# Optimization experiments

Hardware: AMD Instinct MI355X
Metric: run time of the kernel (lower is better)

## Reference

```python
import jax, jax.numpy as jnp
import numpy as np

EMBED_DIM = 512
NUM_HEADS = 8
HEAD_DIM = EMBED_DIM // NUM_HEADS
QK_CH = 64  # hard-coded in the torch module


def setup_inputs() -> dict:
    key = jax.random.key(0)
    ks = jax.random.split(key, 9)
    B, C, H, W = 16, EMBED_DIM, 64, 64
    s = lambda k, shape, fan: jax.random.normal(k, shape, jnp.float32) * (1.0 / np.sqrt(fan))
    return {
        "x": jax.random.normal(ks[0], (B, C, H, W), jnp.float32),
        "Wq": s(ks[1], (QK_CH, C), C),
        "bq": jnp.zeros((QK_CH,), jnp.float32),
        "Wk": s(ks[2], (QK_CH, C), C),
        "bk": jnp.zeros((QK_CH,), jnp.float32),
        "Wv": s(ks[3], (C, C), C),
        "bv": jnp.zeros((C,), jnp.float32),
        "Wo": s(ks[4], (C, C), C),
        "bo": jnp.zeros((C,), jnp.float32),
    }


def reference(x, Wq, bq, Wk, bk, Wv, bv, Wo, bo):
    B, C, H, W = x.shape
    nh, hd = NUM_HEADS, HEAD_DIM
    HW = H * W
    # 1x1 convs == pointwise channel projections
    q = jnp.einsum('bchw,oc->bohw', x, Wq) + bq[None, :, None, None]   # [B,64,H,W]
    k = jnp.einsum('bchw,oc->bohw', x, Wk) + bk[None, :, None, None]   # [B,64,H,W]
    v = jnp.einsum('bchw,oc->bohw', x, Wv) + bv[None, :, None, None]   # [B,C,H,W]
    # split_heads: view(B, nh, -1, hd).permute(0,1,3,2)
    Lq = QK_CH * HW // C
    q = q.reshape(B, nh, Lq, hd).transpose(0, 1, 3, 2)   # [B,nh,hd,Lq]
    k = k.reshape(B, nh, Lq, hd).transpose(0, 1, 3, 2)   # [B,nh,hd,Lq]
    v = v.reshape(B, nh, HW, hd).transpose(0, 1, 3, 2)   # [B,nh,hd,HW]
    # scores: [B,nh,hd,hd], softmax over last dim
    scores = jnp.einsum('bhdl,bhel->bhde', q, k) / np.sqrt(hd).astype(np.float32)
    attn = jax.nn.softmax(scores, axis=-1)
    out = jnp.einsum('bhde,bhen->bhdn', attn, v)          # [B,nh,hd,HW]
    # permute(0,1,3,2).view(B,nh,hd,H,W).permute(0,2,1,3,4).view(B,C,H,W)
    out = out.transpose(0, 1, 3, 2).reshape(B, nh, hd, H, W)
    out = out.transpose(0, 2, 1, 3, 4).reshape(B, C, H, W)
    # output_linear on the flat view [B, HW, C] (plain reshape, as in torch)
    out = out.reshape(B, HW, C) @ Wo.T + bo
    return out.reshape(B, C, H, W)
```

## Files before the change

kernel.cpp:

```cpp
#include <hip/hip_runtime.h>
#include <hip/hip_bf16.h>


#define B_  16
#define C_  512
#define HW_ 4096
#define NO_ 640

typedef unsigned short u16;
typedef __attribute__((ext_vector_type(8))) short bh8;
typedef __attribute__((ext_vector_type(4))) float f32x4;

__device__ __forceinline__ float bf2f(u16 u) {
    unsigned v = ((unsigned)u) << 16;
    return __uint_as_float(v);
}
__device__ __forceinline__ u16 f2bf(float f) {
    unsigned u = __float_as_uint(f);
    unsigned r = (u + 0x7FFFu + ((u >> 16) & 1u)) >> 16;
    return (u16)r;
}

__device__ __forceinline__ void gl2lds(const u16* g, u16* l) {
    __builtin_amdgcn_global_load_lds(
        (const __attribute__((address_space(1))) unsigned int*)(const void*)g,
        (__attribute__((address_space(3))) unsigned int*)(void*)l, 16, 0, 0);
}

__global__ __launch_bounds__(256) void k_wcvt(
    const float* __restrict__ Wq, const float* __restrict__ Wk,
    const float* __restrict__ Wv, const float* __restrict__ Wo,
    u16* __restrict__ Wcat, u16* __restrict__ Wob)
{
    int idx = blockIdx.x * 256 + threadIdx.x;
    if (idx < NO_ * C_) {
        int o = idx >> 9, c = idx & 511;
        float v = (o < 64) ? Wq[o * C_ + c]
                : (o < 128) ? Wk[(o - 64) * C_ + c]
                : Wv[(size_t)(o - 128) * C_ + c];
        Wcat[idx] = f2bf(v);
    }
    int idx2 = idx - NO_ * C_;
    if (idx2 >= 0 && idx2 < C_ * C_) Wob[idx2] = f2bf(Wo[idx2]);
}

__global__ __launch_bounds__(256) void k_x2t(
    const float* __restrict__ x, u16* __restrict__ xT)
{
    __shared__ u16 T[32][33];
    const int t = threadIdx.x;
    const int s0 = blockIdx.x * 32, c0 = blockIdx.y * 32, b = blockIdx.z;
    const float* xb = x + ((size_t)b * C_ + c0) * HW_ + s0;
    {
        int c = t >> 3, s4 = (t & 7) * 4;
        float4 v = *(const float4*)(xb + (size_t)c * HW_ + s4);
        T[s4][c] = f2bf(v.x); T[s4 + 1][c] = f2bf(v.y);
        T[s4 + 2][c] = f2bf(v.z); T[s4 + 3][c] = f2bf(v.w);
    }
    __syncthreads();
    {
        int s = t >> 3, cb = (t & 7) * 4;
        ushort4 o;
        o.x = T[s][cb]; o.y = T[s][cb + 1]; o.z = T[s][cb + 2]; o.w = T[s][cb + 3];
        *(ushort4*)(xT + ((size_t)b * HW_ + s0 + s) * C_ + c0 + cb) = o;
    }
}

__global__ __launch_bounds__(256) void k_proj(
    const u16* __restrict__ Wcat, const u16* __restrict__ xT,
    const float* __restrict__ bq, const float* __restrict__ bk,
    const float* __restrict__ bv, u16* __restrict__ qkv)
{
    __shared__ u16 As[128 * 32];
    __shared__ u16 Bs[128 * 32];
    const int t = threadIdx.x;
    const int lane = t & 63, w = t >> 6;
    const int q = lane >> 4, ln = lane & 15;
    const int n0 = blockIdx.x * 128, m0 = blockIdx.y * 128, b = blockIdx.z;
    const u16* xTb = xT + (size_t)b * HW_ * C_;
    const int wm = (w >> 1) * 64, wn = (w & 1) * 64;
    const int srow = lane >> 2, scol = (lane & 3) * 8;

    f32x4 acc[4][4];
#pragma unroll
    for (int i = 0; i < 4; ++i)
#pragma unroll
        for (int j = 0; j < 4; ++j) acc[i][j] = (f32x4){0.f, 0.f, 0.f, 0.f};

    for (int k0 = 0; k0 < C_; k0 += 32) {
        __syncthreads();
#pragma unroll
        for (int i = 0; i < 2; ++i) {
            int rowblk = (i * 4 + w) * 16;
            gl2lds(Wcat + (size_t)(m0 + rowblk + srow) * C_ + k0 + scol, &As[rowblk * 32]);
            gl2lds(xTb  + (size_t)(n0 + rowblk + srow) * C_ + k0 + scol, &Bs[rowblk * 32]);
        }
        __syncthreads();
        bh8 af[4], bfv[4];
#pragma unroll
        for (int i = 0; i < 4; ++i) af[i]  = *(const bh8*)&As[(wm + i * 16 + ln) * 32 + q * 8];
#pragma unroll
        for (int j = 0; j < 4; ++j) bfv[j] = *(const bh8*)&Bs[(wn + j * 16 + ln) * 32 + q * 8];
#pragma unroll
        for (int i = 0; i < 4; ++i)
#pragma unroll
            for (int j = 0; j < 4; ++j)
                acc[i][j] = __builtin_amdgcn_mfma_f32_16x16x32_bf16(af[i], bfv[j], acc[i][j], 0, 0, 0);
    }

    u16* qb = qkv + (size_t)b * NO_ * HW_;
#pragma unroll
    for (int i = 0; i < 4; ++i) {
#pragma unroll
        for (int r = 0; r < 4; ++r) {
            int o = m0 + wm + i * 16 + q * 4 + r;
            float bia = (o < 64) ? bq[o] : (o < 128) ? bk[o - 64] : bv[o - 128];
#pragma unroll
            for (int j = 0; j < 4; ++j) {
                int s = n0 + wn + j * 16 + ln;
                qb[(size_t)o * HW_ + s] = f2bf(acc[i][j][r] + bia);
            }
        }
    }
}

__global__ __launch_bounds__(256) void k_scores(
    const u16* __restrict__ qkv, float* __restrict__ At)
{
    __shared__ float Ks[64][4];
    __shared__ float Ss[64 * 65];
    const int t = threadIdx.x;
    const int bh = blockIdx.x;
    const int b = bh >> 3, head = bh & 7;
    const int d = t & 63, eg = t >> 6;
    const u16* qbase = qkv + ((size_t)b * NO_ + 8 * head) * HW_;
    const u16* kbase = qkv + ((size_t)b * NO_ + 64 + 8 * head) * HW_;

    float acc[16];
#pragma unroll
    for (int i = 0; i < 16; ++i) acc[i] = 0.f;

    for (int l0 = 0; l0 < 512; l0 += 4) {
        __syncthreads();
        {
            int li = t >> 6, e = t & 63;
            int l = l0 + li;
            Ks[e][li] = bf2f(kbase[(size_t)(l >> 6) * HW_ + ((l & 63) << 6) + e]);
        }
        __syncthreads();
        const u16* ql = qbase + (size_t)(l0 >> 6) * HW_ + ((l0 & 63) << 6) + d;
        float q0 = bf2f(ql[0]), q1 = bf2f(ql[64]), q2 = bf2f(ql[128]), q3 = bf2f(ql[192]);
#pragma unroll
        for (int i = 0; i < 16; ++i) {
            float4 kv = *(const float4*)Ks[eg * 16 + i];
            acc[i] += q0 * kv.x + q1 * kv.y + q2 * kv.z + q3 * kv.w;
        }
    }

    __syncthreads();
#pragma unroll
    for (int i = 0; i < 16; ++i) Ss[d * 65 + eg * 16 + i] = acc[i] * 0.125f;
    __syncthreads();

    if (t < 64) {
        int row = t;
        float m = -1e30f;
        for (int e = 0; e < 64; ++e) m = fmaxf(m, Ss[row * 65 + e]);
        float ssum = 0.f;
        for (int e = 0; e < 64; ++e) {
            float v = __expf(Ss[row * 65 + e] - m);
            Ss[row * 65 + e] = v;
            ssum += v;
        }
        float inv = 1.f / ssum;
        float* Ab = At + (size_t)bh * 4096;
        for (int e = 0; e < 64; ++e) Ab[e * 64 + row] = Ss[row * 65 + e] * inv;
    }
}

__global__ __launch_bounds__(256) void k_apply(
    const u16* __restrict__ qkv, const float* __restrict__ At,
    u16* __restrict__ Xb16)
{
    __shared__ float Ats[4096];
    __shared__ float Vs[4096];
    const int t = threadIdx.x;
    const int a = blockIdx.x, head = blockIdx.y, b = blockIdx.z;
    const float* Ag = At + (size_t)(b * 8 + head) * 4096;
    const u16*   Vg = qkv + ((size_t)b * NO_ + 128 + 64 * head + a) * HW_;

#pragma unroll
    for (int i = 0; i < 4; ++i) {
        int idx = i * 1024 + t * 4;
        *(float4*)&Ats[idx] = *(const float4*)&Ag[idx];
        ushort4 vv = *(const ushort4*)&Vg[idx];
        Vs[idx]     = bf2f(vv.x); Vs[idx + 1] = bf2f(vv.y);
        Vs[idx + 2] = bf2f(vv.z); Vs[idx + 3] = bf2f(vv.w);
    }
    __syncthreads();

    const int w = t & 63, hg = t >> 6;
    float areg[64];
#pragma unroll
    for (int e = 0; e < 64; ++e) areg[e] = Ats[e * 64 + w];

    u16* ob = Xb16 + ((size_t)b * C_ + (a * 8 + head)) * HW_;
    for (int hh = 0; hh < 16; ++hh) {
        int h = hg * 16 + hh;
        float acc = 0.f;
#pragma unroll
        for (int e4 = 0; e4 < 16; ++e4) {
            float4 vv = *(const float4*)&Vs[h * 64 + e4 * 4];
            acc += vv.x * areg[e4 * 4] + vv.y * areg[e4 * 4 + 1]
                 + vv.z * areg[e4 * 4 + 2] + vv.w * areg[e4 * 4 + 3];
        }
        ob[h * 64 + w] = f2bf(acc);
    }
}

__global__ __launch_bounds__(256) void k_out(
    const u16* __restrict__ Xg, const u16* __restrict__ Wob,
    const float* __restrict__ bo, float* __restrict__ Y)
{
    __shared__ u16 As[128 * 32];
    __shared__ u16 Bs[128 * 32];
    const int t = threadIdx.x;
    const int lane = t & 63, w = t >> 6;
    const int q = lane >> 4, ln = lane & 15;
    const int n0 = blockIdx.x * 128;
    const size_t r0 = (size_t)blockIdx.y * 128;
    const int wm = (w >> 1) * 64, wn = (w & 1) * 64;
    const int srow = lane >> 2, scol = (lane & 3) * 8;

    f32x4 acc[4][4];
#pragma unroll
    for (int i = 0; i < 4; ++i)
#pragma unroll
        for (int j = 0; j < 4; ++j) acc[i][j] = (f32x4){0.f, 0.f, 0.f, 0.f};

    for (int k0 = 0; k0 < C_; k0 += 32) {
        __syncthreads();
#pragma unroll
        for (int i = 0; i < 2; ++i) {
            int rowblk = (i * 4 + w) * 16;
            gl2lds(Xg  + (r0 + rowblk + srow) * C_ + k0 + scol, &As[rowblk * 32]);
            gl2lds(Wob + (size_t)(n0 + rowblk + srow) * C_ + k0 + scol, &Bs[rowblk * 32]);
        }
        __syncthreads();
        bh8 af[4], bfv[4];
#pragma unroll
        for (int i = 0; i < 4; ++i) af[i]  = *(const bh8*)&As[(wm + i * 16 + ln) * 32 + q * 8];
#pragma unroll
        for (int j = 0; j < 4; ++j) bfv[j] = *(const bh8*)&Bs[(wn + j * 16 + ln) * 32 + q * 8];
#pragma unroll
        for (int i = 0; i < 4; ++i)
#pragma unroll
            for (int j = 0; j < 4; ++j)
                acc[i][j] = __builtin_amdgcn_mfma_f32_16x16x32_bf16(af[i], bfv[j], acc[i][j], 0, 0, 0);
    }

#pragma unroll
    for (int i = 0; i < 4; ++i) {
#pragma unroll
        for (int r = 0; r < 4; ++r) {
            size_t row = r0 + wm + i * 16 + q * 4 + r;
#pragma unroll
            for (int j = 0; j < 4; ++j) {
                int col = n0 + wn + j * 16 + ln;
                Y[row * C_ + col] = acc[i][j][r] + bo[col];
            }
        }
    }
}

extern "C" void kernel_launch(void* const* d_in, const int* in_sizes, int n_in,
                              void* d_out, int out_size, void* d_ws, size_t ws_size,
                              hipStream_t stream)
{
    const float* x  = (const float*)d_in[0];
    const float* Wq = (const float*)d_in[1];
    const float* bq = (const float*)d_in[2];
    const float* Wk = (const float*)d_in[3];
    const float* bk = (const float*)d_in[4];
    const float* Wv = (const float*)d_in[5];
    const float* bv = (const float*)d_in[6];
    const float* Wo = (const float*)d_in[7];
    const float* bo = (const float*)d_in[8];

    char* ws = (char*)d_ws;
    u16*   xT   = (u16*)ws;
    u16*   Xb16 = (u16*)ws;
    float* At   = (float*)(ws + 67108864);
    u16*   Wcat = (u16*)(ws + 67108864 + 2097152);
    u16*   Wob  = (u16*)(ws + 67108864 + 2097152 + 655360);
    u16*   qkv  = (u16*)d_out;
    float* Y    = (float*)d_out;

    k_wcvt  <<<dim3((NO_ * C_ + C_ * C_ + 255) / 256), 256, 0, stream>>>(Wq, Wk, Wv, Wo, Wcat, Wob);
    k_x2t   <<<dim3(HW_ / 32, C_ / 32, B_), 256, 0, stream>>>(x, xT);
    k_proj  <<<dim3(HW_ / 128, NO_ / 128, B_), 256, 0, stream>>>(Wcat, xT, bq, bk, bv, qkv);
    k_scores<<<dim3(B_ * 8), 256, 0, stream>>>(qkv, At);
    k_apply <<<dim3(64, 8, B_), 256, 0, stream>>>(qkv, At, Xb16);
    k_out   <<<dim3(C_ / 128, (B_ * HW_) / 128), 256, 0, stream>>>(Xb16, Wob, bo, Y);
}
```

Baseline: 562.3 us.

## Compute attention apply with bf16 MFMA and store attention weights as bf16

The scalar FP32 LDS-based attention-apply kernel is replaced by a bf16 MFMA 16x16x32 kernel. Each block now handles 8 spatial rows across all 64 output channels of a head, and it reads V fragments directly from global memory. The softmax output is written as bf16 in row-major form so it can be loaded straight into MFMA B fragments. This removes the FP32 FMA loops and the LDS staging. In exchange, the attention weights lose precision and the output stores are strided across channels.

```diff
diff --git a/kernel.cpp b/kernel.cpp
--- a/kernel.cpp
+++ b/kernel.cpp
@@ -125,7 +125,7 @@
 }
 
 __global__ __launch_bounds__(256) void k_scores(
-    const u16* __restrict__ qkv, float* __restrict__ At)
+    const u16* __restrict__ qkv, u16* __restrict__ Aw)
 {
     __shared__ float Ks[64][4];
     __shared__ float Ss[64 * 65];
@@ -173,48 +173,63 @@
             ssum += v;
         }
         float inv = 1.f / ssum;
-        float* Ab = At + (size_t)bh * 4096;
-        for (int e = 0; e < 64; ++e) Ab[e * 64 + row] = Ss[row * 65 + e] * inv;
+        u16* Ab = Aw + (size_t)bh * 4096;
+        for (int e = 0; e < 64; ++e) Ab[row * 64 + e] = f2bf(Ss[row * 65 + e] * inv);
     }
 }
 
 __global__ __launch_bounds__(256) void k_apply(
-    const u16* __restrict__ qkv, const float* __restrict__ At,
+    const u16* __restrict__ qkv, const u16* __restrict__ Aw,
     u16* __restrict__ Xb16)
 {
-    __shared__ float Ats[4096];
-    __shared__ float Vs[4096];
-    const int t = threadIdx.x;
-    const int a = blockIdx.x, head = blockIdx.y, b = blockIdx.z;
-    const float* Ag = At + (size_t)(b * 8 + head) * 4096;
-    const u16*   Vg = qkv + ((size_t)b * NO_ + 128 + 64 * head + a) * HW_;
-
-#pragma unroll
-    for (int i = 0; i < 4; ++i) {
-        int idx = i * 1024 + t * 4;
-        *(float4*)&Ats[idx] = *(const float4*)&Ag[idx];
-        ushort4 vv = *(const ushort4*)&Vg[idx];
-        Vs[idx]     = bf2f(vv.x); Vs[idx + 1] = bf2f(vv.y);
-        Vs[idx + 2] = bf2f(vv.z); Vs[idx + 3] = bf2f(vv.w);
-    }
-    __syncthreads();
-
-    const int w = t & 63, hg = t >> 6;
-    float areg[64];
-#pragma unroll
-    for (int e = 0; e < 64; ++e) areg[e] = Ats[e * 64 + w];
-
-    u16* ob = Xb16 + ((size_t)b * C_ + (a * 8 + head)) * HW_;
-    for (int hh = 0; hh < 16; ++hh) {
-        int h = hg * 16 + hh;
-        float acc = 0.f;
-#pragma unroll
-        for (int e4 = 0; e4 < 16; ++e4) {
-            float4 vv = *(const float4*)&Vs[h * 64 + e4 * 4];
-            acc += vv.x * areg[e4 * 4] + vv.y * areg[e4 * 4 + 1]
-                 + vv.z * areg[e4 * 4 + 2] + vv.w * areg[e4 * 4 + 3];
-        }
-        ob[h * 64 + w] = f2bf(acc);
+    const int t = threadIdx.x;
+    const int lane = t & 63, wv = t >> 6;
+    const int q = lane >> 4, ln = lane & 15;
+    const int hg = blockIdx.x, head = blockIdx.y, b = blockIdx.z;
+    const u16* Ag = Aw + (size_t)(b * 8 + head) * 4096;
+    const u16* Vg = qkv + ((size_t)b * NO_ + 128 + 64 * head) * HW_;
+    u16* ob = Xb16 + ((size_t)b * C_ + head) * HW_;
+
+    bh8 bfv[4][2];
+#pragma unroll
+    for (int j = 0; j < 4; ++j)
+#pragma unroll
+        for (int ks = 0; ks < 2; ++ks)
+            bfv[j][ks] = *(const bh8*)(Ag + (size_t)(j * 16 + ln) * 64 + ks * 32 + q * 8);
+
+#pragma unroll
+    for (int hi = 0; hi < 2; ++hi) {
+        const int h = hg * 8 + wv * 2 + hi;
+        bh8 af[4][2];
+#pragma unroll
+        for (int i = 0; i < 4; ++i)
+#pragma unroll
+            for (int ks = 0; ks < 2; ++ks)
+                af[i][ks] = *(const bh8*)(Vg + (size_t)(i * 16 + ln) * HW_ + h * 64 + ks * 32 + q * 8);
+
+        f32x4 acc[4][4];
+#pragma unroll
+        for (int i = 0; i < 4; ++i)
+#pragma unroll
+            for (int j = 0; j < 4; ++j) acc[i][j] = (f32x4){0.f, 0.f, 0.f, 0.f};
+#pragma unroll
+        for (int ks = 0; ks < 2; ++ks)
+#pragma unroll
+            for (int i = 0; i < 4; ++i)
+#pragma unroll
+                for (int j = 0; j < 4; ++j)
+                    acc[i][j] = __builtin_amdgcn_mfma_f32_16x16x32_bf16(af[i][ks], bfv[j][ks], acc[i][j], 0, 0, 0);
+
+#pragma unroll
+        for (int i = 0; i < 4; ++i)
+#pragma unroll
+            for (int r = 0; r < 4; ++r) {
+                int a = i * 16 + q * 4 + r;
+                u16* orow = ob + (size_t)a * 8 * HW_ + h * 64;
+#pragma unroll
+                for (int j = 0; j < 4; ++j)
+                    orow[j * 16 + ln] = f2bf(acc[i][j][r]);
+            }
     }
 }
 
@@ -290,7 +305,7 @@
     char* ws = (char*)d_ws;
     u16*   xT   = (u16*)ws;
     u16*   Xb16 = (u16*)ws;
-    float* At   = (float*)(ws + 67108864);
+    u16*   Aw   = (u16*)(ws + 67108864);
     u16*   Wcat = (u16*)(ws + 67108864 + 2097152);
     u16*   Wob  = (u16*)(ws + 67108864 + 2097152 + 655360);
     u16*   qkv  = (u16*)d_out;
@@ -299,7 +314,7 @@
     k_wcvt  <<<dim3((NO_ * C_ + C_ * C_ + 255) / 256), 256, 0, stream>>>(Wq, Wk, Wv, Wo, Wcat, Wob);
     k_x2t   <<<dim3(HW_ / 32, C_ / 32, B_), 256, 0, stream>>>(x, xT);
     k_proj  <<<dim3(HW_ / 128, NO_ / 128, B_), 256, 0, stream>>>(Wcat, xT, bq, bk, bv, qkv);
-    k_scores<<<dim3(B_ * 8), 256, 0, stream>>>(qkv, At);
-    k_apply <<<dim3(64, 8, B_), 256, 0, stream>>>(qkv, At, Xb16);
+    k_scores<<<dim3(B_ * 8), 256, 0, stream>>>(qkv, Aw);
+    k_apply <<<dim3(8, 8, B_), 256, 0, stream>>>(qkv, Aw, Xb16);
     k_out   <<<dim3(C_ / 128, (B_ * HW_) / 128), 256, 0, stream>>>(Xb16, Wob, bo, Y);
 }
```

Measured after the change: 472.6 us. 16.0% less time.
